# Performance work log

Hardware: AMD Instinct MI355X
Metric: run time of the kernel (lower is better)

The kernel has to match this reference:

```python
import jax, jax.numpy as jnp
import numpy as np

B, T, E, H, DH = 8, 1024, 1024, 16, 64

def setup_inputs() -> dict:
    key = jax.random.key(0)
    ks = jax.random.split(key, 5)
    x = jax.random.normal(ks[0], (B, T, E), dtype=jnp.float32)
    Wq = jax.random.normal(ks[1], (H, E, DH), dtype=jnp.float32) * (E ** -0.5)
    Wk = jax.random.normal(ks[2], (H, E, DH), dtype=jnp.float32) * (E ** -0.5)
    Wv = jax.random.normal(ks[3], (H, E, DH), dtype=jnp.float32) * (E ** -0.5)
    Wp = jax.random.normal(ks[4], (E, E), dtype=jnp.float32) * (E ** -0.5)
    bp = jnp.zeros((E,), dtype=jnp.float32)
    return {"x": x, "Wq": Wq, "Wk": Wk, "Wv": Wv, "Wp": Wp, "bp": bp}

def reference(x, Wq, Wk, Wv, Wp, bp):
    # per-head projections (bias-free), vectorized over heads
    q = jnp.einsum('bte,hed->bhtd', x, Wq)
    k = jnp.einsum('bte,hed->bhtd', x, Wk)
    v = jnp.einsum('bte,hed->bhtd', x, Wv)
    scale = DH ** -0.5
    att = jnp.einsum('bhtd,bhsd->bhts', q, k) * scale  # [B,H,T,T]
    causal = jnp.tril(jnp.ones((T, T), dtype=bool))
    att = jnp.where(causal, att, -jnp.inf)
    att = jax.nn.softmax(att, axis=-1)
    # dropout is identity in eval mode
    out = jnp.einsum('bhts,bhsd->bhtd', att, v)
    out = out.transpose(0, 2, 1, 3).reshape(B, T, E)  # concat heads in order
    # proj: torch Linear y = x @ W^T + b
    out = out @ Wp.T + bp
    return out
```

## Files before the change

### kernel.cpp

```cpp
#include <hip/hip_runtime.h>

#define Bsz 8
#define Tsz 1024
#define Esz 1024
#define Hsz 16
#define DHsz 64
#define NQKV 3072

typedef _Float16 f16x8 __attribute__((ext_vector_type(8)));
typedef float f32x4 __attribute__((ext_vector_type(4)));
typedef unsigned short u16x8 __attribute__((ext_vector_type(8)));

__device__ __forceinline__ unsigned short f2h(float f) {
    union { _Float16 h; unsigned short u; } cv;
    cv.h = (_Float16)f;
    return cv.u;
}

__device__ __forceinline__ void async16(const void* g, void* l) {
    __builtin_amdgcn_global_load_lds(
        (const __attribute__((address_space(1))) void*)g,
        (__attribute__((address_space(3))) void*)l, 16, 0, 0);
}

#define MFMA(a, b, c) __builtin_amdgcn_mfma_f32_16x16x32_f16((a), (b), (c), 0, 0, 0)


__global__ void cast_f16_kernel(const float* __restrict__ in, unsigned short* __restrict__ outp) {
    int i = (blockIdx.x * 256 + threadIdx.x) * 4;
    float4 v = *(const float4*)(in + i);
    ushort4 o;
    o.x = f2h(v.x); o.y = f2h(v.y); o.z = f2h(v.z); o.w = f2h(v.w);
    *(ushort4*)(outp + i) = o;
}

__global__ void pack_wqkv_kernel(const float* __restrict__ Wq, const float* __restrict__ Wk,
                                 const float* __restrict__ Wv, unsigned short* __restrict__ Bt) {
    int i = (blockIdx.x * 256 + threadIdx.x) * 4;
    int n = i >> 10;
    int e = i & 1023;
    int which = n >> 10, rem = n & 1023, h = rem >> 6, d = rem & 63;
    const float* W = (which == 0) ? Wq : ((which == 1) ? Wk : Wv);
    const float* src = W + ((size_t)h * Esz + e) * DHsz + d;
    ushort4 o;
    o.x = f2h(src[0]);
    o.y = f2h(src[DHsz]);
    o.z = f2h(src[2 * DHsz]);
    o.w = f2h(src[3 * DHsz]);
    *(ushort4*)(Bt + i) = o;
}

__global__ __launch_bounds__(256) void vtrans_kernel(const unsigned short* __restrict__ QKV,
                                                     unsigned short* __restrict__ VT) {
    __shared__ unsigned int tile[64 * 33];
    const int bh = blockIdx.x, tc = blockIdx.y;
    const int b = bh >> 4, h = bh & 15;
    const int tid = threadIdx.x;
    const unsigned short* src = QKV + ((size_t)(b * Tsz) + tc * 64) * NQKV + 2048 + h * 64;
#pragma unroll
    for (int it = 0; it < 2; ++it) {
        int task = tid + it * 256;
        int row = task >> 3, seg = task & 7;
        u16x8 v = *(const u16x8*)(src + (size_t)row * NQKV + seg * 8);
#pragma unroll
        for (int jj = 0; jj < 4; ++jj)
            tile[row * 33 + seg * 4 + jj] =
                (unsigned int)v[2 * jj] | ((unsigned int)v[2 * jj + 1] << 16);
    }
    __syncthreads();
    unsigned short* dst = VT + (size_t)bh * DHsz * Tsz + tc * 64;
#pragma unroll
    for (int it = 0; it < 2; ++it) {
        int task = tid + it * 256;
        int d = task & 63, tseg = task >> 6;
        int du = d >> 1, hi = d & 1;
        u16x8 v;
#pragma unroll
        for (int j = 0; j < 8; ++j) {
            unsigned int w = tile[(tseg * 8 + j) * 33 + du];
            v[j] = (unsigned short)(hi ? (w >> 16) : (w & 0xffffu));
        }
        *(u16x8*)(dst + (size_t)d * Tsz + tseg * 8) = v;
    }
}

template <int MODE>
__global__ __launch_bounds__(256, 3) void gemm_bt(
    const unsigned short* __restrict__ A,
    const unsigned short* __restrict__ Bt,
    int K, int N,
    unsigned short* __restrict__ c16,
    float* __restrict__ outp, const float* __restrict__ bias)
{
    __shared__ unsigned short smem[17408];
    unsigned short* sA = smem;
    unsigned short* sB = smem + 4096;
    const int tid = threadIdx.x;
    const int wid = tid >> 6, lane = tid & 63;
    const int quad = lane >> 4, l16 = lane & 15;
    const int col0 = blockIdx.x * 128;
    const int row0 = blockIdx.y * 128;
    const int wm = (wid >> 1) * 64, wn = (wid & 1) * 64;

    const f32x4 zero4 = {0.f, 0.f, 0.f, 0.f};
    f32x4 acc[4][4];
#pragma unroll
    for (int i = 0; i < 4; ++i)
#pragma unroll
        for (int j = 0; j < 4; ++j) acc[i][j] = zero4;

    const unsigned short* gA = A + (size_t)row0 * K;
    const unsigned short* gB = Bt + (size_t)col0 * K;
    const int c0 = wid * 2;
    const int srw = lane >> 2;
    const int ssg = (lane & 3) * 8;

    for (int k0 = 0; k0 < K; k0 += 32) {
#pragma unroll
        for (int cc = 0; cc < 2; ++cc) {
            int c = c0 + cc;
            async16(gA + (size_t)(c * 16 + srw) * K + k0 + ssg, (void*)(sA + c * 512 + lane * 8));
            async16(gB + (size_t)(c * 16 + srw) * K + k0 + ssg, (void*)(sB + c * 512 + lane * 8));
        }
        __syncthreads();

        f16x8 af[4], bfr[4];
#pragma unroll
        for (int i = 0; i < 4; ++i)
            af[i] = *(const f16x8*)(sA + (wm + i * 16 + l16) * 32 + quad * 8);
#pragma unroll
        for (int j = 0; j < 4; ++j)
            bfr[j] = *(const f16x8*)(sB + (wn + j * 16 + l16) * 32 + quad * 8);
#pragma unroll
        for (int i = 0; i < 4; ++i)
#pragma unroll
            for (int j = 0; j < 4; ++j)
                acc[i][j] = MFMA(af[i], bfr[j], acc[i][j]);
        __syncthreads();
    }

    if (MODE == 0) {
#pragma unroll
        for (int i = 0; i < 4; ++i)
#pragma unroll
            for (int r = 0; r < 4; ++r) {
                int rowL = wm + i * 16 + quad * 4 + r;
                unsigned short* tr = smem + rowL * 136 + wn + l16;
#pragma unroll
                for (int j = 0; j < 4; ++j)
                    tr[j * 16] = f2h(acc[i][j][r]);
            }
        __syncthreads();
        unsigned short* ob = c16 + (size_t)row0 * N + col0;
#pragma unroll
        for (int it = 0; it < 8; ++it) {
            int rowG = wid * 32 + it * 4 + quad;
            u16x8 v = *(const u16x8*)(smem + rowG * 136 + l16 * 8);
            *(u16x8*)(ob + (size_t)rowG * N + l16 * 8) = v;
        }
    } else {
#pragma unroll
        for (int i = 0; i < 4; ++i) {
            int rb = row0 + wm + i * 16 + quad * 4;
#pragma unroll
            for (int r = 0; r < 4; ++r) {
                float* orow = outp + (size_t)(rb + r) * N;
#pragma unroll
                for (int j = 0; j < 4; ++j) {
                    int c = col0 + wn + j * 16 + l16;
                    orow[c] = acc[i][j][r] + bias[c];
                }
            }
        }
    }
}

__global__ __launch_bounds__(512, 4) void attn_kernel(
    const unsigned short* __restrict__ QKV,
    const unsigned short* __restrict__ VTg,
    unsigned short* __restrict__ AO)
{
    const int bh = blockIdx.x;
    const int pair = blockIdx.y;
    const int b = bh >> 4, h = bh & 15;
    const int tid = threadIdx.x, wid = tid >> 6, lane = tid & 63;
    const int quad = lane >> 4, l16 = lane & 15;

    __shared__ unsigned short sK[64 * 64];
    __shared__ unsigned short sVt[64 * 64];
    __shared__ unsigned short sP[128 * 72];

    const unsigned short* Qb = QKV + (size_t)(b * Tsz) * NQKV + h * 64;
    const unsigned short* Kb = QKV + (size_t)(b * Tsz) * NQKV + 1024 + h * 64;
    const unsigned short* VTb = VTg + (size_t)bh * DHsz * Tsz;

    const int srow = lane >> 3;
    const int sseg = lane & 7;
    const int slog = sseg ^ srow;
    const int r0 = wid * 8;

    const float C1 = 0.18033688f;
    const float C2 = -4.32808512f;
    const f32x4 zero4 = {0.f, 0.f, 0.f, 0.f};

    for (int half = 0; half < 2; ++half) {
        const int qt = (half == 0) ? (7 - pair) : pair;
        const int q0 = qt * 128;
        const int rowlo = q0 + wid * 16;
        const int prow0 = wid * 16;

        f16x8 qf[2];
#pragma unroll
        for (int kk = 0; kk < 2; ++kk)
            qf[kk] = *(const f16x8*)(Qb + (size_t)(rowlo + l16) * NQKV + kk * 32 + quad * 8);

        f32x4 o[4];
        float lp[4];
#pragma unroll
        for (int dt = 0; dt < 4; ++dt) o[dt] = zero4;
#pragma unroll
        for (int r = 0; r < 4; ++r) lp[r] = 0.f;

        const int nblk = (q0 >> 6) + 2;
        for (int blk = 0; blk < nblk; ++blk) {
            const int s0 = blk * 64;
            __syncthreads();
            async16(Kb + (size_t)(s0 + r0 + srow) * NQKV + slog * 8,
                    (void*)(sK + r0 * 64 + lane * 8));
            async16(VTb + (size_t)(r0 + srow) * Tsz + s0 + slog * 8,
                    (void*)(sVt + r0 * 64 + lane * 8));
            __syncthreads();

            if (s0 > rowlo + 15) continue;

            f32x4 sc[4];
#pragma unroll
            for (int ct = 0; ct < 4; ++ct) sc[ct] = zero4;
#pragma unroll
            for (int kk = 0; kk < 2; ++kk) {
                f16x8 kf[4];
#pragma unroll
                for (int ct = 0; ct < 4; ++ct)
                    kf[ct] = *(const f16x8*)(sK + (ct * 16 + l16) * 64 +
                                             (((kk * 4 + quad) ^ (l16 & 7)) * 8));
#pragma unroll
                for (int ct = 0; ct < 4; ++ct)
                    sc[ct] = MFMA(qf[kk], kf[ct], sc[ct]);
            }

            if (s0 + 63 <= rowlo) {
#pragma unroll
                for (int r = 0; r < 4; ++r) {
                    unsigned short* pr = sP + (prow0 + quad * 4 + r) * 72 + l16;
#pragma unroll
                    for (int ct = 0; ct < 4; ++ct) {
                        float p = exp2f(fmaf(sc[ct][r], C1, C2));
                        lp[r] += p;
                        pr[ct * 16] = f2h(p);
                    }
                }
            } else {
#pragma unroll
                for (int r = 0; r < 4; ++r) {
                    int qrow = rowlo + quad * 4 + r;
                    unsigned short* pr = sP + (prow0 + quad * 4 + r) * 72 + l16;
#pragma unroll
                    for (int ct = 0; ct < 4; ++ct) {
                        float p = exp2f(fmaf(sc[ct][r], C1, C2));
                        p = (s0 + ct * 16 + l16 > qrow) ? 0.f : p;
                        lp[r] += p;
                        pr[ct * 16] = f2h(p);
                    }
                }
            }

#pragma unroll
            for (int kk = 0; kk < 2; ++kk) {
                f16x8 pf, vf[4];
                pf = *(const f16x8*)(sP + (prow0 + l16) * 72 + kk * 32 + quad * 8);
#pragma unroll
                for (int dt = 0; dt < 4; ++dt)
                    vf[dt] = *(const f16x8*)(sVt + (dt * 16 + l16) * 64 +
                                             (((kk * 4 + quad) ^ (l16 & 7)) * 8));
#pragma unroll
                for (int dt = 0; dt < 4; ++dt)
                    o[dt] = MFMA(pf, vf[dt], o[dt]);
            }
        }

#pragma unroll
        for (int r = 0; r < 4; ++r) {
            float s = lp[r];
            s += __shfl_xor(s, 1, 64);
            s += __shfl_xor(s, 2, 64);
            s += __shfl_xor(s, 4, 64);
            s += __shfl_xor(s, 8, 64);
            float inv = 1.0f / s;
            unsigned short* orow = sP + (prow0 + quad * 4 + r) * 72 + l16;
#pragma unroll
            for (int dt = 0; dt < 4; ++dt)
                orow[dt * 16] = f2h(o[dt][r] * inv);
        }
#pragma unroll
        for (int it = 0; it < 2; ++it) {
            int r8 = it * 8 + srow;
            u16x8 v = *(const u16x8*)(sP + (prow0 + r8) * 72 + sseg * 8);
            *(u16x8*)(AO + ((size_t)(b * Tsz + q0 + wid * 16 + r8)) * Esz +
                      h * 64 + sseg * 8) = v;
        }
    }
}


extern "C" void kernel_launch(void* const* d_in, const int* in_sizes, int n_in,
                              void* d_out, int out_size, void* d_ws, size_t ws_size,
                              hipStream_t stream)
{
    const float* x  = (const float*)d_in[0];
    const float* Wq = (const float*)d_in[1];
    const float* Wk = (const float*)d_in[2];
    const float* Wv = (const float*)d_in[3];
    const float* Wp = (const float*)d_in[4];
    const float* bp = (const float*)d_in[5];
    float* out = (float*)d_out;

    char* ws = (char*)d_ws;
    unsigned short* xb   = (unsigned short*)(ws);
    unsigned short* wqkv = (unsigned short*)(ws + 16777216);
    unsigned short* wpb  = (unsigned short*)(ws + 23068672);
    unsigned short* qkv  = (unsigned short*)(ws + 25165824);
    unsigned short* ao   = (unsigned short*)(ws + 75497472);
    unsigned short* vtb  = xb;

    cast_f16_kernel<<<8192, 256, 0, stream>>>(x, xb);
    pack_wqkv_kernel<<<3072, 256, 0, stream>>>(Wq, Wk, Wv, wqkv);
    cast_f16_kernel<<<1024, 256, 0, stream>>>(Wp, wpb);

    gemm_bt<0><<<dim3(24, 64), 256, 0, stream>>>(xb, wqkv, 1024, 3072,
                                                 qkv, nullptr, nullptr);

    vtrans_kernel<<<dim3(128, 16), 256, 0, stream>>>(qkv, vtb);

    attn_kernel<<<dim3(128, 4), 512, 0, stream>>>(qkv, vtb, ao);

    gemm_bt<1><<<dim3(8, 64), 256, 0, stream>>>(ao, wpb, 1024, 1024,
                                                nullptr, out, bp);
}
```

Baseline: 257.3 us.

## Retile attention to 64-row query tiles and coalesce weight pack and output stores

Several changes land together. The attention kernel now uses 256-thread blocks on 64-row query tiles with a doubled grid, which drops the skipped-block branch and the wasted K/V loads from the larger tile. The QKV weight pack becomes an LDS-tiled transpose so both its reads and writes are coalesced. The projection GEMM epilogue stages fp32 results through shared memory to issue float4 coalesced stores, and the GEMM occupancy hint is raised from 3 to 4 blocks. The trade-off is more K/V reloads per query row in attention and possible register pressure from the higher occupancy bound.

```diff
diff --git a/kernel.cpp b/kernel.cpp
--- a/kernel.cpp
+++ b/kernel.cpp
@@ -34,20 +34,38 @@
     *(ushort4*)(outp + i) = o;
 }
 
-__global__ void pack_wqkv_kernel(const float* __restrict__ Wq, const float* __restrict__ Wk,
-                                 const float* __restrict__ Wv, unsigned short* __restrict__ Bt) {
-    int i = (blockIdx.x * 256 + threadIdx.x) * 4;
-    int n = i >> 10;
-    int e = i & 1023;
-    int which = n >> 10, rem = n & 1023, h = rem >> 6, d = rem & 63;
+__global__ __launch_bounds__(256) void pack_wqkv_kernel(
+    const float* __restrict__ Wq, const float* __restrict__ Wk,
+    const float* __restrict__ Wv, unsigned short* __restrict__ Bt) {
+    __shared__ unsigned int tile[64 * 33];
+    const int blk = blockIdx.x;
+    const int et = blk & 15, h = (blk >> 4) & 15, which = blk >> 8;
+    const int tid = threadIdx.x;
     const float* W = (which == 0) ? Wq : ((which == 1) ? Wk : Wv);
-    const float* src = W + ((size_t)h * Esz + e) * DHsz + d;
-    ushort4 o;
-    o.x = f2h(src[0]);
-    o.y = f2h(src[DHsz]);
-    o.z = f2h(src[2 * DHsz]);
-    o.w = f2h(src[3 * DHsz]);
-    *(ushort4*)(Bt + i) = o;
+    const float* src = W + ((size_t)h * Esz + et * 64) * DHsz;
+#pragma unroll
+    for (int it = 0; it < 4; ++it) {
+        int task = tid + it * 256;
+        int er = task >> 4, ds = task & 15;
+        float4 v = *(const float4*)(src + (size_t)er * DHsz + ds * 4);
+        tile[er * 33 + ds * 2]     = (unsigned int)f2h(v.x) | ((unsigned int)f2h(v.y) << 16);
+        tile[er * 33 + ds * 2 + 1] = (unsigned int)f2h(v.z) | ((unsigned int)f2h(v.w) << 16);
+    }
+    __syncthreads();
+    unsigned short* dst = Bt + ((size_t)(which * 1024 + h * 64)) * Esz + et * 64;
+#pragma unroll
+    for (int it = 0; it < 2; ++it) {
+        int task = tid + it * 256;
+        int d = task & 63, es = task >> 6;
+        int du = d >> 1, hi = d & 1;
+        u16x8 v;
+#pragma unroll
+        for (int j = 0; j < 8; ++j) {
+            unsigned int w = tile[(es * 8 + j) * 33 + du];
+            v[j] = (unsigned short)(hi ? (w >> 16) : (w & 0xffffu));
+        }
+        *(u16x8*)(dst + (size_t)d * Esz + es * 8) = v;
+    }
 }
 
 __global__ __launch_bounds__(256) void vtrans_kernel(const unsigned short* __restrict__ QKV,
@@ -85,7 +103,7 @@
 }
 
 template <int MODE>
-__global__ __launch_bounds__(256, 3) void gemm_bt(
+__global__ __launch_bounds__(256, 4) void gemm_bt(
     const unsigned short* __restrict__ A,
     const unsigned short* __restrict__ Bt,
     int K, int N,
@@ -159,23 +177,35 @@
             *(u16x8*)(ob + (size_t)rowG * N + l16 * 8) = v;
         }
     } else {
-#pragma unroll
-        for (int i = 0; i < 4; ++i) {
-            int rb = row0 + wm + i * 16 + quad * 4;
-#pragma unroll
-            for (int r = 0; r < 4; ++r) {
-                float* orow = outp + (size_t)(rb + r) * N;
-#pragma unroll
-                for (int j = 0; j < 4; ++j) {
-                    int c = col0 + wn + j * 16 + l16;
-                    orow[c] = acc[i][j][r] + bias[c];
-                }
-            }
-        }
-    }
-}
-
-__global__ __launch_bounds__(512, 4) void attn_kernel(
+        float* ft = (float*)smem;
+#pragma unroll
+        for (int p = 0; p < 2; ++p) {
+            __syncthreads();
+            if ((wid >> 1) == p) {
+#pragma unroll
+                for (int i = 0; i < 4; ++i)
+#pragma unroll
+                    for (int r = 0; r < 4; ++r) {
+                        int rowL = i * 16 + quad * 4 + r;
+                        float* tr = ft + rowL * 136 + wn + l16;
+#pragma unroll
+                        for (int j = 0; j < 4; ++j)
+                            tr[j * 16] = acc[i][j][r] + bias[col0 + wn + j * 16 + l16];
+                    }
+            }
+            __syncthreads();
+#pragma unroll
+            for (int it = 0; it < 8; ++it) {
+                int task = tid + it * 256;
+                int rowL = task >> 5, cs = task & 31;
+                float4 v = *(const float4*)(ft + rowL * 136 + cs * 4);
+                *(float4*)(outp + (size_t)(row0 + p * 64 + rowL) * N + col0 + cs * 4) = v;
+            }
+        }
+    }
+}
+
+__global__ __launch_bounds__(256, 6) void attn_kernel(
     const unsigned short* __restrict__ QKV,
     const unsigned short* __restrict__ VTg,
     unsigned short* __restrict__ AO)
@@ -188,7 +218,7 @@
 
     __shared__ unsigned short sK[64 * 64];
     __shared__ unsigned short sVt[64 * 64];
-    __shared__ unsigned short sP[128 * 72];
+    __shared__ unsigned short sP[64 * 72];
 
     const unsigned short* Qb = QKV + (size_t)(b * Tsz) * NQKV + h * 64;
     const unsigned short* Kb = QKV + (size_t)(b * Tsz) * NQKV + 1024 + h * 64;
@@ -197,15 +227,15 @@
     const int srow = lane >> 3;
     const int sseg = lane & 7;
     const int slog = sseg ^ srow;
-    const int r0 = wid * 8;
+    const int r0 = wid * 16;
 
     const float C1 = 0.18033688f;
     const float C2 = -4.32808512f;
     const f32x4 zero4 = {0.f, 0.f, 0.f, 0.f};
 
     for (int half = 0; half < 2; ++half) {
-        const int qt = (half == 0) ? (7 - pair) : pair;
-        const int q0 = qt * 128;
+        const int qt = (half == 0) ? (15 - pair) : pair;
+        const int q0 = qt * 64;
         const int rowlo = q0 + wid * 16;
         const int prow0 = wid * 16;
 
@@ -221,17 +251,19 @@
 #pragma unroll
         for (int r = 0; r < 4; ++r) lp[r] = 0.f;
 
-        const int nblk = (q0 >> 6) + 2;
+        const int nblk = qt + 1;
         for (int blk = 0; blk < nblk; ++blk) {
             const int s0 = blk * 64;
             __syncthreads();
-            async16(Kb + (size_t)(s0 + r0 + srow) * NQKV + slog * 8,
-                    (void*)(sK + r0 * 64 + lane * 8));
-            async16(VTb + (size_t)(r0 + srow) * Tsz + s0 + slog * 8,
-                    (void*)(sVt + r0 * 64 + lane * 8));
+#pragma unroll
+            for (int ii = 0; ii < 2; ++ii) {
+                int rr = r0 + ii * 8;
+                async16(Kb + (size_t)(s0 + rr + srow) * NQKV + slog * 8,
+                        (void*)(sK + rr * 64 + lane * 8));
+                async16(VTb + (size_t)(rr + srow) * Tsz + s0 + slog * 8,
+                        (void*)(sVt + rr * 64 + lane * 8));
+            }
             __syncthreads();
-
-            if (s0 > rowlo + 15) continue;
 
             f32x4 sc[4];
 #pragma unroll
@@ -248,7 +280,7 @@
                     sc[ct] = MFMA(qf[kk], kf[ct], sc[ct]);
             }
 
-            if (s0 + 63 <= rowlo) {
+            if (blk < nblk - 1) {
 #pragma unroll
                 for (int r = 0; r < 4; ++r) {
                     unsigned short* pr = sP + (prow0 + quad * 4 + r) * 72 + l16;
@@ -333,7 +365,7 @@
     unsigned short* vtb  = xb;
 
     cast_f16_kernel<<<8192, 256, 0, stream>>>(x, xb);
-    pack_wqkv_kernel<<<3072, 256, 0, stream>>>(Wq, Wk, Wv, wqkv);
+    pack_wqkv_kernel<<<768, 256, 0, stream>>>(Wq, Wk, Wv, wqkv);
     cast_f16_kernel<<<1024, 256, 0, stream>>>(Wp, wpb);
 
     gemm_bt<0><<<dim3(24, 64), 256, 0, stream>>>(xb, wqkv, 1024, 3072,
@@ -341,7 +373,7 @@
 
     vtrans_kernel<<<dim3(128, 16), 256, 0, stream>>>(qkv, vtb);
 
-    attn_kernel<<<dim3(128, 4), 512, 0, stream>>>(qkv, vtb, ao);
+    attn_kernel<<<dim3(128, 8), 256, 0, stream>>>(qkv, vtb, ao);
 
     gemm_bt<1><<<dim3(8, 64), 256, 0, stream>>>(ao, wpb, 1024, 1024,
                                                 nullptr, out, bp);
```

Result: slower. 279.1 us (+8.5%).
